# Kernel optimization log

Measured on AMD Instinct MI355X. Metric: run time of the kernel, lower is better.

The kernel has to match this reference:

```python
import jax, jax.numpy as jnp
import numpy as np

B, D, E = 16384, 2048, 16
MIN_K, MAX_K = 1, 4
H = D // 2  # hidden width of similarity/routing MLPs
TOP20 = int(0.2 * D)  # static: int(0.2 * x.shape[-1])


def _lin_init(k, fan_in, shape):
    bound = 1.0 / np.sqrt(fan_in)
    return jax.random.uniform(k, shape, jnp.float32, -bound, bound)


def setup_inputs() -> dict:
    key = jax.random.key(0)
    ks = jax.random.split(key, 16)
    return {
        'x': jax.random.normal(ks[0], (B, D), jnp.float32),
        'expert_patterns': jax.random.normal(ks[1], (E, D), jnp.float32),
        # similarity_network: Linear(D, D//2) -> ReLU -> Linear(D//2, E)
        'Ws1': _lin_init(ks[2], D, (D, H)), 'bs1': _lin_init(ks[3], D, (H,)),
        'Ws2': _lin_init(ks[4], H, (H, E)), 'bs2': _lin_init(ks[5], H, (E,)),
        # routing_network: Linear(D+E, D//2) -> ReLU -> (Dropout eval) -> Linear(D//2, E) -> Softmax
        'Wr1': _lin_init(ks[6], D + E, (D + E, H)), 'br1': _lin_init(ks[7], D + E, (H,)),
        'Wr2': _lin_init(ks[8], H, (H, E)), 'br2': _lin_init(ks[9], H, (E,)),
        # k_predictor: Linear(6,16) -> ReLU -> Linear(16,1) -> Sigmoid
        'Wk1': _lin_init(ks[10], 6, (6, 16)), 'bk1': _lin_init(ks[11], 6, (16,)),
        'Wk2': _lin_init(ks[12], 16, (16, 1)), 'bk2': _lin_init(ks[13], 16, (1,)),
    }


def _feature_analysis(x):
    mean = jnp.mean(x, axis=-1, keepdims=True)
    var_u = jnp.var(x, axis=-1, ddof=1)  # torch.var is unbiased
    std = jnp.sqrt(var_u[:, None] + 1e-8)
    skew = jnp.mean(((x - mean) / std) ** 3, axis=-1)
    ax = jnp.abs(x)
    sorted_ax = -jnp.sort(-ax, axis=-1)  # descending
    total = jnp.sum(sorted_ax, axis=-1)
    top = jnp.sum(sorted_ax[:, :TOP20], axis=-1)
    # stacked in DynamicTopKSelector order: sparsity,variance,magnitude,norm,skewness,concentration
    stats = jnp.stack([
        jnp.mean((x == 0).astype(jnp.float32), axis=-1),
        var_u,
        jnp.max(ax, axis=-1),
        jnp.linalg.norm(x, axis=-1),
        skew,
        top / (total + 1e-8),
    ], axis=-1)  # [B, 6]
    return stats


def _lower_median(v):
    # torch.median returns the lower of two middle elements for even n
    n = v.shape[0]
    return jnp.sort(v)[(n - 1) // 2]


def reference(x, expert_patterns, Ws1, bs1, Ws2, bs2, Wr1, br1, Wr2, br2, Wk1, bk1, Wk2, bk2):
    stats = _feature_analysis(x)  # [B, 6]
    # expert specialization
    sims = x @ expert_patterns.T                                  # [B, E]
    spec = jax.nn.relu(x @ Ws1 + bs1) @ Ws2 + bs2                 # [B, E]
    spec_scores = jax.nn.sigmoid(sims + spec)
    # routing network (dropout inactive in eval)
    ri = jnp.concatenate([x, spec_scores], axis=-1)               # [B, D+E]
    probs = jax.nn.softmax(jax.nn.relu(ri @ Wr1 + br1) @ Wr2 + br2, axis=-1)
    # dynamic top-k (host-side scalar in torch -> static-shape pad/mask here)
    k_ratio = jax.nn.sigmoid(jax.nn.relu(stats @ Wk1 + bk1) @ Wk2 + bk2)[:, 0]
    k_values = MIN_K + (MAX_K - MIN_K) * k_ratio
    k = jnp.clip(jnp.floor(_lower_median(k_values)).astype(jnp.int32), MIN_K, MAX_K)
    k = jax.lax.stop_gradient(k)
    topk_probs, topk_idx = jax.lax.top_k(probs, MAX_K)            # [B, MAX_K]
    mask = jnp.arange(MAX_K) < k                                  # first k slots active
    gates = jax.nn.softmax(jnp.where(mask, topk_probs, -1e30), axis=-1)
    return gates, topk_idx, probs, stats
```

## Files before the change

kernel.cpp:

```cpp
#include <hip/hip_runtime.h>
#include <hip/hip_bf16.h>

typedef unsigned short u16;
typedef __attribute__((ext_vector_type(8))) short bf16x8;
typedef __attribute__((ext_vector_type(8))) unsigned short u16x8;
typedef __attribute__((ext_vector_type(4))) float f32x4;

#define BB 16384
#define DD 2048
#define KEXT 2112
#define HH 1024
#define EE 16
#define TOPN 409

__device__ __forceinline__ u16 f2bf(float f) {
    union { float f; unsigned u; } c; c.f = f;
    unsigned r = c.u + 0x7fffu + ((c.u >> 16) & 1u);
    return (u16)(r >> 16);
}
__device__ __forceinline__ float bf2f(u16 h) {
    union { unsigned u; float f; } c; c.u = ((unsigned)h) << 16; return c.f;
}

__device__ __forceinline__ void ld16_lds(const void* g, void* l) {
    __builtin_amdgcn_global_load_lds(
        (const __attribute__((address_space(1))) unsigned int*)g,
        (__attribute__((address_space(3))) unsigned int*)l, 16, 0, 0);
}

__global__ __launch_bounds__(256)
void prep_t(const float* __restrict__ Ws1, const float* __restrict__ Wr1,
            u16* __restrict__ w1t, u16* __restrict__ wr1h, u16* __restrict__ wr1l)
{
    __shared__ float tile[64][65];
    const int kt = blockIdx.x;
    const int nt = blockIdx.y;
    const int mat = blockIdx.z;
    if (mat == 0 && kt >= 32) return;
    const int k0 = kt * 64, n0 = nt * 64;
    const float* src = mat ? Wr1 : Ws1;
    const int kmax = mat ? (DD + EE) : DD;
    const int t = threadIdx.x;
    #pragma unroll
    for (int i = 0; i < 16; ++i) {
        int e = i * 256 + t;
        int r = e >> 6, c = e & 63;
        float v = (k0 + r < kmax) ? src[(size_t)(k0 + r) * HH + n0 + c] : 0.0f;
        tile[r][c] = v;
    }
    __syncthreads();
    #pragma unroll
    for (int i = 0; i < 16; ++i) {
        int e = i * 256 + t;
        int rn = e >> 6, ck = e & 63;
        float v = tile[ck][rn];
        size_t oidx = (size_t)(n0 + rn) * KEXT + k0 + ck;
        if (mat == 0) {
            w1t[oidx] = f2bf(v);
        } else {
            u16 h = f2bf(v);
            wr1h[oidx] = h;
            wr1l[oidx] = f2bf(v - bf2f(h));
        }
    }
}

__global__ __launch_bounds__(256)
void prep_small(const float* __restrict__ Ws2, const float* __restrict__ Wr2,
                const float* __restrict__ pat,
                u16* __restrict__ w2t1, u16* __restrict__ wr2th, u16* __restrict__ wr2tl,
                u16* __restrict__ patTh, u16* __restrict__ patTl)
{
    int idx = blockIdx.x * 256 + threadIdx.x;
    if (idx < EE * HH) {
        int e = idx / HH, n = idx % HH;
        w2t1[idx] = f2bf(Ws2[(size_t)n * EE + e]);
        float v = Wr2[(size_t)n * EE + e];
        u16 h = f2bf(v);
        wr2th[idx] = h;
        wr2tl[idx] = f2bf(v - bf2f(h));
    }
    if (idx < EE * DD) {
        float v = pat[idx];
        u16 h = f2bf(v);
        patTh[idx] = h;
        patTl[idx] = f2bf(v - bf2f(h));
    }
}

__global__ __launch_bounds__(256)
void stats_kernel(const float* __restrict__ x,
                  const float* __restrict__ Wk1, const float* __restrict__ bk1,
                  const float* __restrict__ Wk2, const float* __restrict__ bk2,
                  float* __restrict__ stats_out, u16* __restrict__ xh, u16* __restrict__ xl,
                  unsigned* __restrict__ kflags)
{
    const int wid = threadIdx.x >> 6;
    const int lane = threadIdx.x & 63;
    const int row = blockIdx.x * 4 + wid;
    const float* xr = x + (size_t)row * DD;

    float v[32];
    #pragma unroll
    for (int s = 0; s < 8; ++s) {
        float4 a = *(const float4*)(xr + s * 256 + lane * 4);
        v[s*4+0]=a.x; v[s*4+1]=a.y; v[s*4+2]=a.z; v[s*4+3]=a.w;
    }

    u16* ph = xh + (size_t)row * KEXT;
    u16* pl = xl + (size_t)row * KEXT;
    #pragma unroll
    for (int s = 0; s < 8; ++s) {
        union { u16 a[4]; unsigned long long q; } H, L;
        #pragma unroll
        for (int c = 0; c < 4; ++c) {
            float f = v[s*4+c];
            u16 h = f2bf(f);
            H.a[c] = h; L.a[c] = f2bf(f - bf2f(h));
        }
        *(unsigned long long*)(ph + s*256 + lane*4) = H.q;
        *(unsigned long long*)(pl + s*256 + lane*4) = L.q;
    }
    ph[DD + lane] = 0;
    pl[DD + lane] = 0;

    float s1 = 0;
    #pragma unroll
    for (int j = 0; j < 32; ++j) s1 += v[j];
    #pragma unroll
    for (int off = 32; off >= 1; off >>= 1) s1 += __shfl_xor(s1, off);
    const float mean = s1 * (1.0f/2048.0f);

    float s2=0, s3=0, sa=0, sq=0, zc=0, mx=0;
    #pragma unroll
    for (int j = 0; j < 32; ++j) {
        float d = v[j] - mean;
        s2 += d*d; s3 += d*d*d;
        float av = fabsf(v[j]);
        sa += av; sq += v[j]*v[j];
        mx = fmaxf(mx, av);
        zc += (v[j] == 0.0f) ? 1.0f : 0.0f;
    }
    #pragma unroll
    for (int off = 32; off >= 1; off >>= 1) {
        s2 += __shfl_xor(s2, off);
        s3 += __shfl_xor(s3, off);
        sa += __shfl_xor(sa, off);
        sq += __shfl_xor(sq, off);
        zc += __shfl_xor(zc, off);
        mx = fmaxf(mx, __shfl_xor(mx, off));
    }

    #pragma unroll
    for (int j = 0; j < 32; ++j) v[j] = fabsf(v[j]);

    unsigned lo = 0, hi = 0x7F800000u;
    while (lo < hi) {
        unsigned mid = (lo + hi) >> 1;
        float midf = __uint_as_float(mid);
        unsigned cnt = 0;
        #pragma unroll
        for (int j = 0; j < 32; ++j)
            cnt += (unsigned)__popcll(__ballot(v[j] > midf));
        if (cnt < TOPN) hi = mid; else lo = mid + 1;
    }
    const float T = __uint_as_float(lo);

    float cg = 0, sg = 0;
    #pragma unroll
    for (int j = 0; j < 32; ++j) {
        if (v[j] > T) { cg += 1.0f; sg += v[j]; }
    }
    #pragma unroll
    for (int off = 32; off >= 1; off >>= 1) { cg += __shfl_xor(cg, off); sg += __shfl_xor(sg, off); }

    if (lane == 0) {
        float top = sg + ((float)TOPN - cg) * T;
        float var_u = s2 * (1.0f/2047.0f);
        float stdv = sqrtf(var_u + 1e-8f);
        float st0 = zc * (1.0f/2048.0f);
        float st1 = var_u;
        float st2 = mx;
        float st3 = sqrtf(sq);
        float st4 = (s3 * (1.0f/2048.0f)) / (stdv*stdv*stdv);
        float st5 = top / (sa + 1e-8f);
        float* so = stats_out + (size_t)row * 6;
        so[0]=st0; so[1]=st1; so[2]=st2; so[3]=st3; so[4]=st4; so[5]=st5;
        float stv[6] = {st0,st1,st2,st3,st4,st5};
        float o = bk2[0];
        #pragma unroll
        for (int i = 0; i < 16; ++i) {
            float h = bk1[i];
            #pragma unroll
            for (int f = 0; f < 6; ++f) h += stv[f] * Wk1[f*16 + i];
            o += fmaxf(h, 0.0f) * Wk2[i];
        }
        float kr = 1.0f / (1.0f + expf(-o));
        float kv = 1.0f + 3.0f * kr;
        kflags[row] = (kv < 2.0f ? 1u : 0u) | (kv < 3.0f ? 0x10000u : 0u);
    }
}

__global__ __launch_bounds__(1024)
void kmed_kernel(const unsigned* __restrict__ kflags, int* __restrict__ counters)
{
    const int t = threadIdx.x;
    unsigned s = 0;
    for (int i = t; i < BB; i += 1024) s += kflags[i];
    #pragma unroll
    for (int off = 32; off >= 1; off >>= 1) s += __shfl_xor(s, off);
    __shared__ unsigned red[16];
    if ((t & 63) == 0) red[t >> 6] = s;
    __syncthreads();
    if (t == 0) {
        unsigned tot = 0;
        #pragma unroll
        for (int w = 0; w < 16; ++w) tot += red[w];
        counters[0] = (int)(tot & 0xFFFFu);
        counters[1] = (int)(tot >> 16);
    }
}

template<bool SPLIT3, bool OSPLIT>
__global__ __launch_bounds__(256)
void gemm_tile(const u16* __restrict__ Ah, const u16* __restrict__ Al,
               const u16* __restrict__ Bh, const u16* __restrict__ Bl,
               const float* __restrict__ bias,
               u16* __restrict__ Oh, u16* __restrict__ Ol,
               int kiters, int stride)
{
    __shared__ u16 AsH[128*64];
    __shared__ u16 BsH[128*64];
    __shared__ u16 AsL[SPLIT3 ? 128*64 : 8];
    __shared__ u16 BsL[SPLIT3 ? 128*64 : 8];
    const int t = threadIdx.x;
    const int id = blockIdx.x;
    const int xcd = id & 7;
    const int jj = id >> 3;
    const int nblk = jj & 7;
    const int mgrp = jj >> 3;
    const int m0 = (xcd * 16 + mgrp) * 128;
    const int n0 = nblk * 128;
    const int wid = t >> 6, lane = t & 63, l16 = lane & 15, q = lane >> 4;
    const int wm = (wid & 1) * 64, wn = (wid >> 1) * 64;
    const int x7 = l16 & 7;

    f32x4 acc[4][4] = {};

    for (int it = 0; it < kiters; ++it) {
        const int k0 = it * 64;
        __syncthreads();
        #pragma unroll
        for (int s = 0; s < 4; ++s) {
            int seg = t + s * 256;
            int row = seg >> 3;
            int c = (seg & 7) ^ (row & 7);
            size_t goff = (size_t)k0 + c * 8;
            size_t aoff = (size_t)(m0 + row) * stride + goff;
            size_t boff = (size_t)(n0 + row) * stride + goff;
            ld16_lds(Ah + aoff, (void*)(AsH + seg * 8));
            ld16_lds(Bh + boff, (void*)(BsH + seg * 8));
            if constexpr (SPLIT3) {
                ld16_lds(Al + aoff, (void*)(AsL + seg * 8));
                ld16_lds(Bl + boff, (void*)(BsL + seg * 8));
            }
        }
        __syncthreads();
        #pragma unroll
        for (int h = 0; h < 2; ++h) {
            const int coff = ((4*h + q) ^ x7) * 8;
            bf16x8 afh[4], bfh[4], afl[4], bfl[4];
            #pragma unroll
            for (int i = 0; i < 4; ++i) {
                const int ra = (wm + 16*i + l16) * 64 + coff;
                const int rb = (wn + 16*i + l16) * 64 + coff;
                afh[i] = *(const bf16x8*)(AsH + ra);
                bfh[i] = *(const bf16x8*)(BsH + rb);
                if constexpr (SPLIT3) {
                    afl[i] = *(const bf16x8*)(AsL + ra);
                    bfl[i] = *(const bf16x8*)(BsL + rb);
                }
            }
            #pragma unroll
            for (int i = 0; i < 4; ++i)
                #pragma unroll
                for (int j = 0; j < 4; ++j) {
                    acc[i][j] = __builtin_amdgcn_mfma_f32_16x16x32_bf16(afh[i], bfh[j], acc[i][j], 0, 0, 0);
                    if constexpr (SPLIT3) {
                        acc[i][j] = __builtin_amdgcn_mfma_f32_16x16x32_bf16(afh[i], bfl[j], acc[i][j], 0, 0, 0);
                        acc[i][j] = __builtin_amdgcn_mfma_f32_16x16x32_bf16(afl[i], bfh[j], acc[i][j], 0, 0, 0);
                    }
                }
        }
    }
    #pragma unroll
    for (int j = 0; j < 4; ++j) {
        int col = n0 + wn + 16*j + l16;
        float bv = bias[col];
        #pragma unroll
        for (int i = 0; i < 4; ++i)
            #pragma unroll
            for (int r = 0; r < 4; ++r) {
                int row = m0 + wm + 16*i + q*4 + r;
                float vv = acc[i][j][r] + bv;
                vv = vv > 0.0f ? vv : 0.0f;
                u16 h = f2bf(vv);
                Oh[(size_t)row * HH + col] = h;
                if constexpr (OSPLIT) Ol[(size_t)row * HH + col] = f2bf(vv - bf2f(h));
            }
    }
}

__global__ __launch_bounds__(256)
void thinA(const u16* __restrict__ xh, const u16* __restrict__ xl,
           const u16* __restrict__ patTh, const u16* __restrict__ patTl,
           const u16* __restrict__ ha, const u16* __restrict__ w2t,
           const float* __restrict__ bs2,
           u16* __restrict__ xh_w, u16* __restrict__ xl_w)
{
    const int t = threadIdx.x;
    const int wid = t >> 6, lane = t & 63, l16 = lane & 15, q = lane >> 4;
    const int m0 = blockIdx.x * 16;
    f32x4 acc = {};
    for (int it = wid; it < 64; it += 4) {
        const int k0 = it * 32;
        bf16x8 a0 = *(const bf16x8*)(xh + (size_t)(m0 + l16) * KEXT + k0 + q*8);
        bf16x8 a1 = *(const bf16x8*)(xl + (size_t)(m0 + l16) * KEXT + k0 + q*8);
        bf16x8 b0 = *(const bf16x8*)(patTh + (size_t)l16 * DD + k0 + q*8);
        bf16x8 b1 = *(const bf16x8*)(patTl + (size_t)l16 * DD + k0 + q*8);
        acc = __builtin_amdgcn_mfma_f32_16x16x32_bf16(a0, b0, acc, 0, 0, 0);
        acc = __builtin_amdgcn_mfma_f32_16x16x32_bf16(a0, b1, acc, 0, 0, 0);
        acc = __builtin_amdgcn_mfma_f32_16x16x32_bf16(a1, b0, acc, 0, 0, 0);
    }
    for (int it = wid; it < 32; it += 4) {
        const int k0 = it * 32;
        bf16x8 a = *(const bf16x8*)(ha + (size_t)(m0 + l16) * HH + k0 + q*8);
        bf16x8 b = *(const bf16x8*)(w2t + (size_t)l16 * HH + k0 + q*8);
        acc = __builtin_amdgcn_mfma_f32_16x16x32_bf16(a, b, acc, 0, 0, 0);
    }
    __shared__ f32x4 red[4][64];
    red[wid][lane] = acc;
    __syncthreads();
    if (wid == 0) {
        f32x4 v = red[0][lane];
        #pragma unroll
        for (int w = 1; w < 4; ++w) {
            f32x4 o = red[w][lane];
            v[0]+=o[0]; v[1]+=o[1]; v[2]+=o[2]; v[3]+=o[3];
        }
        const float b2 = bs2[l16];
        #pragma unroll
        for (int r = 0; r < 4; ++r) {
            int row = m0 + q*4 + r;
            float ssv = 1.0f / (1.0f + expf(-(v[r] + b2)));
            u16 h = f2bf(ssv);
            u16 lo = f2bf(ssv - bf2f(h));
            xh_w[(size_t)row * KEXT + DD + l16] = h;
            xl_w[(size_t)row * KEXT + DD + l16] = lo;
        }
    }
}

__global__ __launch_bounds__(256)
void thinB(const u16* __restrict__ hh, const u16* __restrict__ hl,
           const u16* __restrict__ wr2th, const u16* __restrict__ wr2tl,
           const float* __restrict__ br2, const int* __restrict__ counters,
           float* __restrict__ out_gates, float* __restrict__ out_idx,
           float* __restrict__ out_probs)
{
    const int t = threadIdx.x;
    const int wid = t >> 6, lane = t & 63, l16 = lane & 15, q = lane >> 4;
    const int m0 = blockIdx.x * 16;
    f32x4 acc = {};
    for (int it = wid; it < 32; it += 4) {
        const int k0 = it * 32;
        bf16x8 a0 = *(const bf16x8*)(hh + (size_t)(m0 + l16) * HH + k0 + q*8);
        bf16x8 a1 = *(const bf16x8*)(hl + (size_t)(m0 + l16) * HH + k0 + q*8);
        bf16x8 b0 = *(const bf16x8*)(wr2th + (size_t)l16 * HH + k0 + q*8);
        bf16x8 b1 = *(const bf16x8*)(wr2tl + (size_t)l16 * HH + k0 + q*8);
        acc = __builtin_amdgcn_mfma_f32_16x16x32_bf16(a0, b0, acc, 0, 0, 0);
        acc = __builtin_amdgcn_mfma_f32_16x16x32_bf16(a0, b1, acc, 0, 0, 0);
        acc = __builtin_amdgcn_mfma_f32_16x16x32_bf16(a1, b0, acc, 0, 0, 0);
    }
    __shared__ f32x4 red[4][64];
    red[wid][lane] = acc;
    __syncthreads();
    if (wid != 0) return;
    f32x4 v = red[0][lane];
    #pragma unroll
    for (int w = 1; w < 4; ++w) {
        f32x4 o = red[w][lane];
        v[0]+=o[0]; v[1]+=o[1]; v[2]+=o[2]; v[3]+=o[3];
    }
    const float b2 = br2[l16];
    const int c2 = counters[0], c3 = counters[1];
    const int k = (c2 >= 8192) ? 1 : ((c3 >= 8192) ? 2 : 3);
    #pragma unroll
    for (int r = 0; r < 4; ++r) {
        const int row = m0 + q*4 + r;
        float lg = v[r] + b2;
        float mxv = lg;
        #pragma unroll
        for (int off = 1; off < 16; off <<= 1) mxv = fmaxf(mxv, __shfl_xor(mxv, off));
        float e = expf(lg - mxv);
        float den = e;
        #pragma unroll
        for (int off = 1; off < 16; off <<= 1) den += __shfl_xor(den, off);
        float p = e / den;
        out_probs[(size_t)row * EE + l16] = p;
        int kcur = (int)((__float_as_uint(p) & ~15u) | (15u - (unsigned)l16));
        float tv[4]; int ti[4];
        #pragma unroll
        for (int s = 0; s < 4; ++s) {
            int kk = kcur;
            #pragma unroll
            for (int off = 1; off < 16; off <<= 1) kk = max(kk, __shfl_xor(kk, off));
            int widx = 15 - (kk & 15);
            ti[s] = widx;
            tv[s] = __shfl(p, q * 16 + widx);
            if (l16 == widx) kcur = 0;
        }
        float den2 = 0.0f;
        float g[4];
        #pragma unroll
        for (int s = 0; s < 4; ++s) {
            g[s] = expf(tv[s] - tv[0]);
            if (s < k) den2 += g[s];
        }
        if (l16 < 4) {
            out_gates[(size_t)row * 4 + l16] = (l16 < k) ? g[l16] / den2 : 0.0f;
            out_idx[(size_t)row * 4 + l16] = (float)ti[l16];
        }
    }
}

extern "C" void kernel_launch(void* const* d_in, const int* in_sizes, int n_in,
                              void* d_out, int out_size, void* d_ws, size_t ws_size,
                              hipStream_t stream) {
    const float* x   = (const float*)d_in[0];
    const float* pat = (const float*)d_in[1];
    const float* Ws1 = (const float*)d_in[2];
    const float* bs1 = (const float*)d_in[3];
    const float* Ws2 = (const float*)d_in[4];
    const float* bs2 = (const float*)d_in[5];
    const float* Wr1 = (const float*)d_in[6];
    const float* br1 = (const float*)d_in[7];
    const float* Wr2 = (const float*)d_in[8];
    const float* br2 = (const float*)d_in[9];
    const float* Wk1 = (const float*)d_in[10];
    const float* bk1 = (const float*)d_in[11];
    const float* Wk2 = (const float*)d_in[12];
    const float* bk2 = (const float*)d_in[13];

    char* ws = (char*)d_ws;
    size_t off = 0;
    auto alloc = [&](size_t bytes) { char* p = ws + off; off += (bytes + 255) & ~(size_t)255; return p; };
    u16* xh     = (u16*)alloc((size_t)BB * KEXT * 2);
    u16* xl     = (u16*)alloc((size_t)BB * KEXT * 2);
    u16* w1t    = (u16*)alloc((size_t)HH * KEXT * 2);
    u16* wr1h   = (u16*)alloc((size_t)HH * KEXT * 2);
    u16* wr1l   = (u16*)alloc((size_t)HH * KEXT * 2);
    u16* w2t1   = (u16*)alloc((size_t)EE * HH * 2);
    u16* wr2th  = (u16*)alloc((size_t)EE * HH * 2);
    u16* wr2tl  = (u16*)alloc((size_t)EE * HH * 2);
    u16* patTh  = (u16*)alloc((size_t)EE * DD * 2);
    u16* patTl  = (u16*)alloc((size_t)EE * DD * 2);
    u16* ha     = (u16*)alloc((size_t)BB * HH * 2);
    u16* hb     = (u16*)alloc((size_t)BB * HH * 2);
    unsigned* kflags = (unsigned*)alloc((size_t)BB * 4);
    int* cnt      = (int*)alloc(64);

    float* out        = (float*)d_out;
    float* out_gates  = out;
    float* out_idx    = out + (size_t)BB * 4;
    float* out_probs  = out + (size_t)BB * 8;
    float* out_stats  = out + (size_t)BB * 24;

    prep_t<<<dim3(33, 16, 2), 256, 0, stream>>>(Ws1, Wr1, w1t, wr1h, wr1l);

    prep_small<<<(EE*DD + 255)/256, 256, 0, stream>>>(Ws2, Wr2, pat,
        w2t1, wr2th, wr2tl, patTh, patTl);

    stats_kernel<<<BB/4, 256, 0, stream>>>(x, Wk1, bk1, Wk2, bk2, out_stats, xh, xl, kflags);

    kmed_kernel<<<1, 1024, 0, stream>>>(kflags, cnt);

    gemm_tile<false, false><<<1024, 256, 0, stream>>>(
        xh, nullptr, w1t, nullptr, bs1, ha, nullptr, 32, KEXT);

    thinA<<<BB/16, 256, 0, stream>>>(xh, xl, patTh, patTl, ha, w2t1, bs2, xh, xl);

    gemm_tile<true, true><<<1024, 256, 0, stream>>>(
        xh, xl, wr1h, wr1l, br1, ha, hb, 33, KEXT);

    thinB<<<BB/16, 256, 0, stream>>>(ha, hb, wr2th, wr2tl, br2, cnt,
                                     out_gates, out_idx, out_probs);
}
```

Baseline: 617.4 us.

## Rewrite hidden-layer GEMMs as 256x256-tile software-pipelined kernel with concatenated split-K segments

Replaces the 128x128 single-buffered GEMM with a 512-thread kernel computing 256x256 output tiles. It uses a four-slot LDS ring of 32-wide K slices, explicit vmcnt/lgkmcnt waits, barriers and setprio so that global-to-LDS loads overlap the MFMA work. The three-term bf16 split product is now expressed as one long K loop over concatenated segments (hi*hi, hi*lo, lo*hi, plus one padding tile from lo*lo) instead of three MFMAs per fragment. In exchange, the LDS layout is no longer swizzled, so bank conflicts are possible, and the larger tiles give fewer blocks to fill the GPU.

```diff
diff --git a/kernel.cpp b/kernel.cpp
--- a/kernel.cpp
+++ b/kernel.cpp
@@ -3,7 +3,6 @@
 
 typedef unsigned short u16;
 typedef __attribute__((ext_vector_type(8))) short bf16x8;
-typedef __attribute__((ext_vector_type(8))) unsigned short u16x8;
 typedef __attribute__((ext_vector_type(4))) float f32x4;
 
 #define BB 16384
@@ -221,93 +220,135 @@
     }
 }
 
-template<bool SPLIT3, bool OSPLIT>
-__global__ __launch_bounds__(256)
-void gemm_tile(const u16* __restrict__ Ah, const u16* __restrict__ Al,
-               const u16* __restrict__ Bh, const u16* __restrict__ Bl,
-               const float* __restrict__ bias,
-               u16* __restrict__ Oh, u16* __restrict__ Ol,
-               int kiters, int stride)
-{
-    __shared__ u16 AsH[128*64];
-    __shared__ u16 BsH[128*64];
-    __shared__ u16 AsL[SPLIT3 ? 128*64 : 8];
-    __shared__ u16 BsL[SPLIT3 ? 128*64 : 8];
+#define GBAR()  { asm volatile("" ::: "memory"); __builtin_amdgcn_s_barrier(); asm volatile("" ::: "memory"); }
+#define GLGKM() { asm volatile("s_waitcnt lgkmcnt(0)" ::: "memory"); __builtin_amdgcn_sched_barrier(0); }
+#define GVM8()  { asm volatile("s_waitcnt vmcnt(8)" ::: "memory"); }
+
+template<bool OSPLIT>
+__global__ __launch_bounds__(512, 2)
+void gemm8(const u16* __restrict__ A0, const u16* __restrict__ A1,
+           const u16* __restrict__ A2, const u16* __restrict__ A3,
+           const u16* __restrict__ B0, const u16* __restrict__ B1,
+           const u16* __restrict__ B2, const u16* __restrict__ B3,
+           const float* __restrict__ bias,
+           u16* __restrict__ Oh, u16* __restrict__ Ol,
+           int ntiles, int seglen)
+{
+    __shared__ u16 As[4 * 8192];
+    __shared__ u16 Bs[4 * 8192];
     const int t = threadIdx.x;
+    const int lane = t & 63, wid = t >> 6;
+    const int l16 = lane & 15, q = lane >> 4;
+    const int wmi = wid >> 2, wni = wid & 3;
+
     const int id = blockIdx.x;
     const int xcd = id & 7;
     const int jj = id >> 3;
-    const int nblk = jj & 7;
-    const int mgrp = jj >> 3;
-    const int m0 = (xcd * 16 + mgrp) * 128;
-    const int n0 = nblk * 128;
-    const int wid = t >> 6, lane = t & 63, l16 = lane & 15, q = lane >> 4;
-    const int wm = (wid & 1) * 64, wn = (wid >> 1) * 64;
-    const int x7 = l16 & 7;
-
-    f32x4 acc[4][4] = {};
-
-    for (int it = 0; it < kiters; ++it) {
-        const int k0 = it * 64;
-        __syncthreads();
-        #pragma unroll
-        for (int s = 0; s < 4; ++s) {
-            int seg = t + s * 256;
-            int row = seg >> 3;
-            int c = (seg & 7) ^ (row & 7);
-            size_t goff = (size_t)k0 + c * 8;
-            size_t aoff = (size_t)(m0 + row) * stride + goff;
-            size_t boff = (size_t)(n0 + row) * stride + goff;
-            ld16_lds(Ah + aoff, (void*)(AsH + seg * 8));
-            ld16_lds(Bh + boff, (void*)(BsH + seg * 8));
-            if constexpr (SPLIT3) {
-                ld16_lds(Al + aoff, (void*)(AsL + seg * 8));
-                ld16_lds(Bl + boff, (void*)(BsL + seg * 8));
-            }
-        }
-        __syncthreads();
-        #pragma unroll
-        for (int h = 0; h < 2; ++h) {
-            const int coff = ((4*h + q) ^ x7) * 8;
-            bf16x8 afh[4], bfh[4], afl[4], bfl[4];
+    const int nblk = jj & 3, mgrp = jj >> 2;
+    const int m0 = (xcd * 8 + mgrp) * 256;
+    const int n0 = nblk * 256;
+
+    float bv[4];
+    #pragma unroll
+    for (int j = 0; j < 4; ++j) bv[j] = bias[n0 + wni*64 + 16*j + l16];
+
+    f32x4 acc[8][4] = {};
+    bf16x8 af[4], bfr[4];
+
+    auto stage = [&](int kt, int ks, int slot, bool isB) {
+        if (kt > ntiles - 1) kt = ntiles - 1;
+        const int seg = (kt >= seglen) + (kt >= 2*seglen) + (kt >= 3*seglen);
+        const int kk = kt - seg * seglen;
+        const int kcol = kk * 64 + ks * 32;
+        const u16* sa = seg == 0 ? A0 : seg == 1 ? A1 : seg == 2 ? A2 : A3;
+        const u16* sb = seg == 0 ? B0 : seg == 1 ? B1 : seg == 2 ? B2 : B3;
+        const u16* src = isB ? sb : sa;
+        const int base = isB ? n0 : m0;
+        u16* dst = (isB ? Bs : As) + slot * 8192;
+        #pragma unroll
+        for (int r = 0; r < 2; ++r) {
+            const int idx = t + r * 512;
+            const int row = idx >> 2, c = idx & 3;
+            ld16_lds(src + (size_t)(base + row) * KEXT + kcol + c * 8,
+                     (void*)(dst + idx * 8));
+        }
+    };
+    auto readB4 = [&](int slot) {
+        const u16* s = Bs + slot * 8192;
+        #pragma unroll
+        for (int j = 0; j < 4; ++j) {
+            const int row = wni * 64 + 16 * j + l16;
+            bfr[j] = *(const bf16x8*)(s + row * 32 + q * 8);
+        }
+    };
+    auto readA4 = [&](int slot, int mh) {
+        const u16* s = As + slot * 8192;
+        #pragma unroll
+        for (int ii = 0; ii < 4; ++ii) {
+            const int row = wmi * 128 + mh * 64 + 16 * ii + l16;
+            af[ii] = *(const bf16x8*)(s + row * 32 + q * 8);
+        }
+    };
+    auto mfma16 = [&](int mh) {
+        __builtin_amdgcn_s_setprio(1);
+        #pragma unroll
+        for (int ii = 0; ii < 4; ++ii)
             #pragma unroll
-            for (int i = 0; i < 4; ++i) {
-                const int ra = (wm + 16*i + l16) * 64 + coff;
-                const int rb = (wn + 16*i + l16) * 64 + coff;
-                afh[i] = *(const bf16x8*)(AsH + ra);
-                bfh[i] = *(const bf16x8*)(BsH + rb);
-                if constexpr (SPLIT3) {
-                    afl[i] = *(const bf16x8*)(AsL + ra);
-                    bfl[i] = *(const bf16x8*)(BsL + rb);
-                }
-            }
-            #pragma unroll
-            for (int i = 0; i < 4; ++i)
-                #pragma unroll
-                for (int j = 0; j < 4; ++j) {
-                    acc[i][j] = __builtin_amdgcn_mfma_f32_16x16x32_bf16(afh[i], bfh[j], acc[i][j], 0, 0, 0);
-                    if constexpr (SPLIT3) {
-                        acc[i][j] = __builtin_amdgcn_mfma_f32_16x16x32_bf16(afh[i], bfl[j], acc[i][j], 0, 0, 0);
-                        acc[i][j] = __builtin_amdgcn_mfma_f32_16x16x32_bf16(afl[i], bfh[j], acc[i][j], 0, 0, 0);
-                    }
-                }
-        }
-    }
+            for (int j = 0; j < 4; ++j)
+                acc[mh*4+ii][j] = __builtin_amdgcn_mfma_f32_16x16x32_bf16(
+                    af[ii], bfr[j], acc[mh*4+ii][j], 0, 0, 0);
+        __builtin_amdgcn_s_setprio(0);
+    };
+
+    stage(0, 0, 0, false); stage(0, 0, 0, true);
+    stage(0, 1, 1, false); stage(0, 1, 1, true);
+    stage(1, 0, 2, false); stage(1, 0, 2, true);
+    GVM8(); GBAR();
+
+    const int niter = ntiles >> 1;
+    for (int i = 0; i < niter; ++i) {
+        const int tE = 2*i, tO = 2*i + 1;
+        readB4(0); readA4(0, 0);
+        stage(tO, 1, 3, false);
+        GBAR(); GLGKM(); mfma16(0); GBAR();
+        readA4(0, 1);
+        stage(tO, 1, 3, true);
+        GBAR(); GLGKM(); mfma16(1); GVM8(); GBAR();
+        readB4(1); readA4(1, 0);
+        stage(tE + 2, 0, 0, false);
+        GBAR(); GLGKM(); mfma16(0); GBAR();
+        readA4(1, 1);
+        stage(tE + 2, 0, 0, true);
+        GBAR(); GLGKM(); mfma16(1); GVM8(); GBAR();
+        readB4(2); readA4(2, 0);
+        stage(tE + 2, 1, 1, false);
+        GBAR(); GLGKM(); mfma16(0); GBAR();
+        readA4(2, 1);
+        stage(tE + 2, 1, 1, true);
+        GBAR(); GLGKM(); mfma16(1); GVM8(); GBAR();
+        readB4(3); readA4(3, 0);
+        stage(tO + 2, 0, 2, false);
+        GBAR(); GLGKM(); mfma16(0); GBAR();
+        readA4(3, 1);
+        stage(tO + 2, 0, 2, true);
+        GBAR(); GLGKM(); mfma16(1); GVM8(); GBAR();
+    }
+
     #pragma unroll
     for (int j = 0; j < 4; ++j) {
-        int col = n0 + wn + 16*j + l16;
-        float bv = bias[col];
-        #pragma unroll
-        for (int i = 0; i < 4; ++i)
+        const int col = n0 + wni*64 + 16*j + l16;
+        #pragma unroll
+        for (int i = 0; i < 8; ++i) {
             #pragma unroll
             for (int r = 0; r < 4; ++r) {
-                int row = m0 + wm + 16*i + q*4 + r;
-                float vv = acc[i][j][r] + bv;
+                const int row = m0 + wmi*128 + 16*i + q*4 + r;
+                float vv = acc[i][j][r] + bv[j];
                 vv = vv > 0.0f ? vv : 0.0f;
                 u16 h = f2bf(vv);
                 Oh[(size_t)row * HH + col] = h;
                 if constexpr (OSPLIT) Ol[(size_t)row * HH + col] = f2bf(vv - bf2f(h));
             }
+        }
     }
 }
 
@@ -485,13 +526,13 @@
 
     kmed_kernel<<<1, 1024, 0, stream>>>(kflags, cnt);
 
-    gemm_tile<false, false><<<1024, 256, 0, stream>>>(
-        xh, nullptr, w1t, nullptr, bs1, ha, nullptr, 32, KEXT);
+    gemm8<false><<<256, 512, 0, stream>>>(
+        xh, xh, xh, xh, w1t, w1t, w1t, w1t, bs1, ha, nullptr, 32, 33);
 
     thinA<<<BB/16, 256, 0, stream>>>(xh, xl, patTh, patTl, ha, w2t1, bs2, xh, xl);
 
-    gemm_tile<true, true><<<1024, 256, 0, stream>>>(
-        xh, xl, wr1h, wr1l, br1, ha, hb, 33, KEXT);
+    gemm8<true><<<256, 512, 0, stream>>>(
+        xh, xh, xl, xl, wr1h, wr1l, wr1h, wr1l, br1, ha, hb, 100, 33);
 
     thinB<<<BB/16, 256, 0, stream>>>(ha, hb, wr2th, wr2tl, br2, cnt,
                                      out_gates, out_idx, out_probs);
```

Result: slower. 906.9 us (+46.9%).

## Fuse second similarity-MLP layer into first GEMM epilogue and merge prep kernels

Applied to the files above, without the earlier changes.

The first GEMM's epilogue now stages its ReLU output tile in shared memory and multiplies it by the Ws2 slice with MFMA. It writes per-N-block partial spec sums, so the 32MB hidden activation is never written to global memory and thinA no longer reads it back. thinA then adds the 8 partials before the sigmoid. prep_small is folded into prep_t as an extra z-slice, removing one launch. The trade-off is extra LDS traffic and syncs in the GEMM epilogue, plus the partial-sum buffer aliased onto hb.

```diff
diff --git a/kernel.cpp b/kernel.cpp
--- a/kernel.cpp
+++ b/kernel.cpp
@@ -3,7 +3,6 @@
 
 typedef unsigned short u16;
 typedef __attribute__((ext_vector_type(8))) short bf16x8;
-typedef __attribute__((ext_vector_type(8))) unsigned short u16x8;
 typedef __attribute__((ext_vector_type(4))) float f32x4;
 
 #define BB 16384
@@ -30,17 +29,39 @@
 
 __global__ __launch_bounds__(256)
 void prep_t(const float* __restrict__ Ws1, const float* __restrict__ Wr1,
-            u16* __restrict__ w1t, u16* __restrict__ wr1h, u16* __restrict__ wr1l)
+            u16* __restrict__ w1t, u16* __restrict__ wr1h, u16* __restrict__ wr1l,
+            const float* __restrict__ Ws2, const float* __restrict__ Wr2,
+            const float* __restrict__ pat,
+            u16* __restrict__ w2t1, u16* __restrict__ wr2th, u16* __restrict__ wr2tl,
+            u16* __restrict__ patTh, u16* __restrict__ patTl)
 {
     __shared__ float tile[64][65];
     const int kt = blockIdx.x;
     const int nt = blockIdx.y;
     const int mat = blockIdx.z;
+    const int t = threadIdx.x;
+    if (mat == 2) {
+        int idx = (kt * 16 + nt) * 256 + t;
+        if (idx < EE * HH) {
+            int e = idx / HH, n = idx % HH;
+            w2t1[idx] = f2bf(Ws2[(size_t)n * EE + e]);
+            float v = Wr2[(size_t)n * EE + e];
+            u16 h = f2bf(v);
+            wr2th[idx] = h;
+            wr2tl[idx] = f2bf(v - bf2f(h));
+        }
+        if (idx < EE * DD) {
+            float v = pat[idx];
+            u16 h = f2bf(v);
+            patTh[idx] = h;
+            patTl[idx] = f2bf(v - bf2f(h));
+        }
+        return;
+    }
     if (mat == 0 && kt >= 32) return;
     const int k0 = kt * 64, n0 = nt * 64;
     const float* src = mat ? Wr1 : Ws1;
     const int kmax = mat ? (DD + EE) : DD;
-    const int t = threadIdx.x;
     #pragma unroll
     for (int i = 0; i < 16; ++i) {
         int e = i * 256 + t;
@@ -62,29 +83,6 @@
             wr1h[oidx] = h;
             wr1l[oidx] = f2bf(v - bf2f(h));
         }
-    }
-}
-
-__global__ __launch_bounds__(256)
-void prep_small(const float* __restrict__ Ws2, const float* __restrict__ Wr2,
-                const float* __restrict__ pat,
-                u16* __restrict__ w2t1, u16* __restrict__ wr2th, u16* __restrict__ wr2tl,
-                u16* __restrict__ patTh, u16* __restrict__ patTl)
-{
-    int idx = blockIdx.x * 256 + threadIdx.x;
-    if (idx < EE * HH) {
-        int e = idx / HH, n = idx % HH;
-        w2t1[idx] = f2bf(Ws2[(size_t)n * EE + e]);
-        float v = Wr2[(size_t)n * EE + e];
-        u16 h = f2bf(v);
-        wr2th[idx] = h;
-        wr2tl[idx] = f2bf(v - bf2f(h));
-    }
-    if (idx < EE * DD) {
-        float v = pat[idx];
-        u16 h = f2bf(v);
-        patTh[idx] = h;
-        patTl[idx] = f2bf(v - bf2f(h));
     }
 }
 
@@ -221,18 +219,20 @@
     }
 }
 
-template<bool SPLIT3, bool OSPLIT>
+template<bool SPLIT3, bool OSPLIT, bool FUSE_SPEC>
 __global__ __launch_bounds__(256)
 void gemm_tile(const u16* __restrict__ Ah, const u16* __restrict__ Al,
                const u16* __restrict__ Bh, const u16* __restrict__ Bl,
                const float* __restrict__ bias,
                u16* __restrict__ Oh, u16* __restrict__ Ol,
+               const u16* __restrict__ w2t, float* __restrict__ spec_part,
                int kiters, int stride)
 {
-    __shared__ u16 AsH[128*64];
-    __shared__ u16 BsH[128*64];
-    __shared__ u16 AsL[SPLIT3 ? 128*64 : 8];
-    __shared__ u16 BsL[SPLIT3 ? 128*64 : 8];
+    __shared__ u16 SM[SPLIT3 ? 4*8192 : 2*8192];
+    u16* AsH = SM;
+    u16* BsH = SM + 8192;
+    u16* AsL = SPLIT3 ? SM + 2*8192 : SM;
+    u16* BsL = SPLIT3 ? SM + 3*8192 : SM;
     const int t = threadIdx.x;
     const int id = blockIdx.x;
     const int xcd = id & 7;
@@ -293,28 +293,67 @@
                 }
         }
     }
-    #pragma unroll
-    for (int j = 0; j < 4; ++j) {
-        int col = n0 + wn + 16*j + l16;
-        float bv = bias[col];
-        #pragma unroll
-        for (int i = 0; i < 4; ++i)
+
+    if constexpr (FUSE_SPEC) {
+        __syncthreads();
+        u16* h1t = SM;
+        #pragma unroll
+        for (int j = 0; j < 4; ++j) {
+            int col = wn + 16*j + l16;
+            float bvj = bias[n0 + col];
+            #pragma unroll
+            for (int i = 0; i < 4; ++i)
+                #pragma unroll
+                for (int r = 0; r < 4; ++r) {
+                    int row = wm + 16*i + q*4 + r;
+                    float vv = acc[i][j][r] + bvj;
+                    vv = vv > 0.0f ? vv : 0.0f;
+                    h1t[row * 128 + col] = f2bf(vv);
+                }
+        }
+        __syncthreads();
+        const int mb = wid * 32;
+        f32x4 s16[2] = {};
+        #pragma unroll
+        for (int kk = 0; kk < 4; ++kk) {
+            bf16x8 wb = *(const bf16x8*)(w2t + (size_t)l16 * HH + n0 + kk*32 + q*8);
+            #pragma unroll
+            for (int i2 = 0; i2 < 2; ++i2) {
+                bf16x8 af = *(const bf16x8*)(h1t + (mb + i2*16 + l16) * 128 + kk*32 + q*8);
+                s16[i2] = __builtin_amdgcn_mfma_f32_16x16x32_bf16(af, wb, s16[i2], 0, 0, 0);
+            }
+        }
+        #pragma unroll
+        for (int i2 = 0; i2 < 2; ++i2)
             #pragma unroll
             for (int r = 0; r < 4; ++r) {
-                int row = m0 + wm + 16*i + q*4 + r;
-                float vv = acc[i][j][r] + bv;
-                vv = vv > 0.0f ? vv : 0.0f;
-                u16 h = f2bf(vv);
-                Oh[(size_t)row * HH + col] = h;
-                if constexpr (OSPLIT) Ol[(size_t)row * HH + col] = f2bf(vv - bf2f(h));
+                int row = m0 + mb + i2*16 + q*4 + r;
+                spec_part[((size_t)nblk * BB + row) * EE + l16] = s16[i2][r];
             }
+    } else {
+        #pragma unroll
+        for (int j = 0; j < 4; ++j) {
+            int col = n0 + wn + 16*j + l16;
+            float bv = bias[col];
+            #pragma unroll
+            for (int i = 0; i < 4; ++i)
+                #pragma unroll
+                for (int r = 0; r < 4; ++r) {
+                    int row = m0 + wm + 16*i + q*4 + r;
+                    float vv = acc[i][j][r] + bv;
+                    vv = vv > 0.0f ? vv : 0.0f;
+                    u16 h = f2bf(vv);
+                    Oh[(size_t)row * HH + col] = h;
+                    if constexpr (OSPLIT) Ol[(size_t)row * HH + col] = f2bf(vv - bf2f(h));
+                }
+        }
     }
 }
 
 __global__ __launch_bounds__(256)
 void thinA(const u16* __restrict__ xh, const u16* __restrict__ xl,
            const u16* __restrict__ patTh, const u16* __restrict__ patTl,
-           const u16* __restrict__ ha, const u16* __restrict__ w2t,
+           const float* __restrict__ spec_part,
            const float* __restrict__ bs2,
            u16* __restrict__ xh_w, u16* __restrict__ xl_w)
 {
@@ -332,12 +371,6 @@
         acc = __builtin_amdgcn_mfma_f32_16x16x32_bf16(a0, b1, acc, 0, 0, 0);
         acc = __builtin_amdgcn_mfma_f32_16x16x32_bf16(a1, b0, acc, 0, 0, 0);
     }
-    for (int it = wid; it < 32; it += 4) {
-        const int k0 = it * 32;
-        bf16x8 a = *(const bf16x8*)(ha + (size_t)(m0 + l16) * HH + k0 + q*8);
-        bf16x8 b = *(const bf16x8*)(w2t + (size_t)l16 * HH + k0 + q*8);
-        acc = __builtin_amdgcn_mfma_f32_16x16x32_bf16(a, b, acc, 0, 0, 0);
-    }
     __shared__ f32x4 red[4][64];
     red[wid][lane] = acc;
     __syncthreads();
@@ -352,7 +385,11 @@
         #pragma unroll
         for (int r = 0; r < 4; ++r) {
             int row = m0 + q*4 + r;
-            float ssv = 1.0f / (1.0f + expf(-(v[r] + b2)));
+            float sp = 0.0f;
+            #pragma unroll
+            for (int p = 0; p < 8; ++p)
+                sp += spec_part[((size_t)p * BB + row) * EE + l16];
+            float ssv = 1.0f / (1.0f + expf(-(v[r] + sp + b2)));
             u16 h = f2bf(ssv);
             u16 lo = f2bf(ssv - bf2f(h));
             xh_w[(size_t)row * KEXT + DD + l16] = h;
@@ -470,28 +507,28 @@
     unsigned* kflags = (unsigned*)alloc((size_t)BB * 4);
     int* cnt      = (int*)alloc(64);
 
+    float* spec_part = (float*)hb;
+
     float* out        = (float*)d_out;
     float* out_gates  = out;
     float* out_idx    = out + (size_t)BB * 4;
     float* out_probs  = out + (size_t)BB * 8;
     float* out_stats  = out + (size_t)BB * 24;
 
-    prep_t<<<dim3(33, 16, 2), 256, 0, stream>>>(Ws1, Wr1, w1t, wr1h, wr1l);
-
-    prep_small<<<(EE*DD + 255)/256, 256, 0, stream>>>(Ws2, Wr2, pat,
-        w2t1, wr2th, wr2tl, patTh, patTl);
+    prep_t<<<dim3(33, 16, 3), 256, 0, stream>>>(Ws1, Wr1, w1t, wr1h, wr1l,
+        Ws2, Wr2, pat, w2t1, wr2th, wr2tl, patTh, patTl);
 
     stats_kernel<<<BB/4, 256, 0, stream>>>(x, Wk1, bk1, Wk2, bk2, out_stats, xh, xl, kflags);
 
     kmed_kernel<<<1, 1024, 0, stream>>>(kflags, cnt);
 
-    gemm_tile<false, false><<<1024, 256, 0, stream>>>(
-        xh, nullptr, w1t, nullptr, bs1, ha, nullptr, 32, KEXT);
-
-    thinA<<<BB/16, 256, 0, stream>>>(xh, xl, patTh, patTl, ha, w2t1, bs2, xh, xl);
-
-    gemm_tile<true, true><<<1024, 256, 0, stream>>>(
-        xh, xl, wr1h, wr1l, br1, ha, hb, 33, KEXT);
+    gemm_tile<false, false, true><<<1024, 256, 0, stream>>>(
+        xh, nullptr, w1t, nullptr, bs1, nullptr, nullptr, w2t1, spec_part, 32, KEXT);
+
+    thinA<<<BB/16, 256, 0, stream>>>(xh, xl, patTh, patTl, spec_part, bs2, xh, xl);
+
+    gemm_tile<true, true, false><<<1024, 256, 0, stream>>>(
+        xh, xl, wr1h, wr1l, br1, ha, hb, nullptr, nullptr, 33, KEXT);
 
     thinB<<<BB/16, 256, 0, stream>>>(ha, hb, wr2th, wr2tl, br2, cnt,
                                      out_gates, out_idx, out_probs);
```

After: 610.5 us. No clear change (-1.1%).
